# Kernel tuning notes

Hardware: AMD Instinct MI355X
Metric: run time of the kernel (lower is better)

The kernel has to match this reference:

```python
import jax, jax.numpy as jnp
import numpy as np

B, N, D, H = 16, 256, 1024, 8
DK = D // H
WAVE_LEN = 1000.0


def box_relational_embedding(boxes):
    # boxes: (B, N, 4) as (x_min, y_min, x_max, y_max)
    x_min, y_min, x_max, y_max = jnp.split(boxes, 4, axis=-1)  # each (B, N, 1)
    cx = (x_min + x_max) * 0.5
    cy = (y_min + y_max) * 0.5
    w = (x_max - x_min) + 1.0
    h = (y_max - y_min) + 1.0
    # pairwise deltas (B, N, N); row i = query box, col j = key box
    delta_x = jnp.log(jnp.clip(jnp.abs((cx - jnp.swapaxes(cx, -2, -1)) / w), 1e-3, None))
    delta_y = jnp.log(jnp.clip(jnp.abs((cy - jnp.swapaxes(cy, -2, -1)) / h), 1e-3, None))
    delta_w = jnp.log(w / jnp.swapaxes(w, -2, -1))
    delta_h = jnp.log(h / jnp.swapaxes(h, -2, -1))
    pos = jnp.stack([delta_x, delta_y, delta_w, delta_h], axis=-1)  # (B, N, N, 4)
    # sinusoidal expansion: dim_g = 64 -> 8 frequencies per delta
    feat_range = jnp.arange(8, dtype=pos.dtype) / 8.0
    dim_mat = 1.0 / (WAVE_LEN ** feat_range)  # (8,)
    mul = (100.0 * pos)[..., None] * dim_mat  # (B, N, N, 4, 8)
    mul = mul.reshape(pos.shape[:3] + (32,))
    return jnp.concatenate([jnp.sin(mul), jnp.cos(mul)], axis=-1)  # (B, N, N, 64)


def setup_inputs() -> dict:
    key = jax.random.key(0)
    ks = jax.random.split(key, 12)
    x = jax.random.normal(ks[0], (B, N, D), dtype=jnp.float32)
    # valid boxes: x_max > x_min, y_max > y_min
    xy = jax.random.uniform(ks[1], (B, N, 2), dtype=jnp.float32) * 100.0
    wh = jax.random.uniform(ks[2], (B, N, 2), dtype=jnp.float32) * 50.0 + 1.0
    boxes = jnp.concatenate([xy, xy + wh], axis=-1)
    s = 1.0 / np.sqrt(D)
    Wq = jax.random.normal(ks[3], (D, D), dtype=jnp.float32) * s
    Wk = jax.random.normal(ks[4], (D, D), dtype=jnp.float32) * s
    Wv = jax.random.normal(ks[5], (D, D), dtype=jnp.float32) * s
    Wo = jax.random.normal(ks[6], (D, D), dtype=jnp.float32) * s
    bq = jnp.zeros((D,), jnp.float32)
    bk = jnp.zeros((D,), jnp.float32)
    bv = jnp.zeros((D,), jnp.float32)
    bo = jnp.zeros((D,), jnp.float32)
    Wg = jax.random.normal(ks[7], (H, 64), dtype=jnp.float32) * (1.0 / 8.0)  # 8 per-head (64->1) linears
    bg = jnp.zeros((H,), jnp.float32)
    return {"x": x, "boxes": boxes, "Wq": Wq, "bq": bq, "Wk": Wk, "bk": bk,
            "Wv": Wv, "bv": bv, "Wo": Wo, "bo": bo, "Wg": Wg, "bg": bg}


def reference(x, boxes, Wq, bq, Wk, bk, Wv, bv, Wo, bo, Wg, bg):
    emb = box_relational_embedding(boxes)  # (B, N, N, 64)
    # per-head geometric weights, ReLU'd: (B, H, N, N)
    geo = jax.nn.relu(jnp.einsum('bnmg,hg->bhnm', emb, Wg) + bg[None, :, None, None])
    q = (x @ Wq + bq).reshape(B, N, H, DK).transpose(0, 2, 1, 3)  # (B, H, N, DK)
    k = (x @ Wk + bk).reshape(B, N, H, DK).transpose(0, 2, 1, 3)
    v = (x @ Wv + bv).reshape(B, N, H, DK).transpose(0, 2, 1, 3)
    scores = jnp.einsum('bhnd,bhmd->bhnm', q, k) / np.sqrt(DK)
    w_mn = jax.nn.softmax(jnp.log(jnp.clip(geo, 1e-6, None)) + scores, axis=-1)
    out = jnp.einsum('bhnm,bhmd->bhnd', w_mn, v)  # (B, H, N, DK)
    out = out.transpose(0, 2, 1, 3).reshape(B, N, D)
    return out @ Wo + bo
```

## Files before the change

kernel.cpp:

```cpp
#include <hip/hip_runtime.h>

#define Bb 16
#define Nn 256
#define Dd 1024
#define Hh 8
#define DKk 128

typedef unsigned short u16;
typedef __attribute__((ext_vector_type(8))) short bfrag;
typedef __attribute__((ext_vector_type(4))) float f4;

#define MFMA16(a, b, c) __builtin_amdgcn_mfma_f32_16x16x32_bf16((a), (b), (c), 0, 0, 0)

__device__ __forceinline__ u16 f2b(float f) {
  unsigned int u = __builtin_bit_cast(unsigned int, f);
  u += 0x7fffu + ((u >> 16) & 1u);
  return (u16)(u >> 16);
}

typedef __attribute__((address_space(1))) void GV;
typedef __attribute__((address_space(3))) void LV;
__device__ __forceinline__ void gload16(const void* g, void* l) {
  __builtin_amdgcn_global_load_lds((GV*)g, (LV*)l, 16, 0, 0);
}

__global__ __launch_bounds__(256) void cast_x_kernel(const float* __restrict__ x,
                                                     u16* __restrict__ xb) {
  const int i = blockIdx.x * 256 + threadIdx.x;
  const float4 v = ((const float4*)x)[i];
  union { u16 u[4]; unsigned long long ll; } p;
  p.u[0] = f2b(v.x); p.u[1] = f2b(v.y); p.u[2] = f2b(v.z); p.u[3] = f2b(v.w);
  ((unsigned long long*)xb)[i] = p.ll;
}

__global__ __launch_bounds__(256) void transpose_w_kernel(
    const float* __restrict__ Wq, const float* __restrict__ Wk,
    const float* __restrict__ Wv, const float* __restrict__ Wo,
    u16* __restrict__ wqkvt, u16* __restrict__ wot) {
  __shared__ float t[32][33];
  const int bid = blockIdx.x;
  const int which = bid >> 10;
  const int tr = (bid >> 5) & 31;
  const int tc = bid & 31;
  const float* W = which == 0 ? Wq : which == 1 ? Wk : which == 2 ? Wv : Wo;
  u16* dst = (which == 3) ? wot : (wqkvt + (long long)which * 1024 * 1024);
  const int tx = threadIdx.x & 31, ty = threadIdx.x >> 5;
#pragma unroll
  for (int rr = 0; rr < 4; rr++)
    t[ty + rr * 8][tx] = W[(tr * 32 + ty + rr * 8) * 1024 + tc * 32 + tx];
  __syncthreads();
#pragma unroll
  for (int rr = 0; rr < 4; rr++)
    dst[(tc * 32 + ty + rr * 8) * 1024 + tr * 32 + tx] = f2b(t[tx][ty + rr * 8]);
}

__global__ __launch_bounds__(256) void transpose_v_kernel(const u16* __restrict__ v,
                                                          u16* __restrict__ vT) {
  __shared__ u16 t[32][33];
  const int bid = blockIdx.x;
  const int bh = bid >> 5;
  const int kt = (bid >> 2) & 7;
  const int ct = bid & 3;
  const u16* src = v + (long long)bh * Nn * DKk;
  u16* dst = vT + (long long)bh * DKk * Nn;
  const int tx = threadIdx.x & 31, ty = threadIdx.x >> 5;
#pragma unroll
  for (int rr = 0; rr < 4; rr++)
    t[ty + rr * 8][tx] = src[(kt * 32 + ty + rr * 8) * DKk + ct * 32 + tx];
  __syncthreads();
#pragma unroll
  for (int rr = 0; rr < 4; rr++)
    dst[(ct * 32 + ty + rr * 8) * Nn + kt * 32 + tx] = t[tx][ty + rr * 8];
}

__global__ __launch_bounds__(256) void geo_kernel(const float* __restrict__ boxes,
                                                  const float* __restrict__ Wg,
                                                  const float* __restrict__ bg,
                                                  float* __restrict__ logg) {
  __shared__ float wg_s[512];
  __shared__ float bg_s[8];
  const int tid = threadIdx.x;
  wg_s[tid] = Wg[tid];
  wg_s[tid + 256] = Wg[tid + 256];
  if (tid < 8) bg_s[tid] = bg[tid];
  __syncthreads();
  const int bid = blockIdx.x;
  const int b = bid >> 8, i = bid & 255;
  const int j = tid;
  const float4 bi4 = ((const float4*)boxes)[b * 256 + i];
  const float4 bj4 = ((const float4*)boxes)[b * 256 + j];
  const float cxi = (bi4.x + bi4.z) * 0.5f, cyi = (bi4.y + bi4.w) * 0.5f;
  const float wi = bi4.z - bi4.x + 1.f, hi = bi4.w - bi4.y + 1.f;
  const float cxj = (bj4.x + bj4.z) * 0.5f, cyj = (bj4.y + bj4.w) * 0.5f;
  const float wj = bj4.z - bj4.x + 1.f, hj = bj4.w - bj4.y + 1.f;
  float pos[4];
  pos[0] = __logf(fmaxf(fabsf((cxi - cxj) / wi), 1e-3f));
  pos[1] = __logf(fmaxf(fabsf((cyi - cyj) / hi), 1e-3f));
  pos[2] = __logf(wi / wj);
  pos[3] = __logf(hi / hj);
  const float dimm[8] = {1.0f, 0.42169650342f, 0.177827941f, 0.0749894209f,
                         0.0316227766f, 0.01333521432f, 0.00562341325f, 0.00237137371f};
  float sv[32], cv[32];
#pragma unroll
  for (int d = 0; d < 4; d++)
#pragma unroll
    for (int f = 0; f < 8; f++) {
      const float ang = 100.f * pos[d] * dimm[f];
      __sincosf(ang, &sv[d * 8 + f], &cv[d * 8 + f]);
    }
  const long long base = ((long long)(b * 8) * 256 + i) * 256 + j;
#pragma unroll
  for (int h = 0; h < 8; h++) {
    float a = bg_s[h];
#pragma unroll
    for (int t = 0; t < 32; t++)
      a = fmaf(sv[t], wg_s[h * 64 + t], fmaf(cv[t], wg_s[h * 64 + 32 + t], a));
    logg[base + (long long)h * 65536] = __logf(fmaxf(a, 1e-6f));
  }
}

template <int MODE>
__global__ __launch_bounds__(256) void gemm128(
    const u16* __restrict__ A, const u16* __restrict__ Bt,
    const float* __restrict__ b0, const float* __restrict__ b1,
    const float* __restrict__ b2, u16* __restrict__ oq, u16* __restrict__ ok,
    u16* __restrict__ ov, float* __restrict__ co, int M, int Np, int K) {
  __shared__ u16 As[128 * 32];
  __shared__ u16 Bs[128 * 32];
  const int tilesN = Np >> 7;
  const int bm = blockIdx.x / tilesN, bn = blockIdx.x - bm * tilesN;
  const int m0 = bm << 7, n0 = bn << 7;
  const int tid = threadIdx.x, lane = tid & 63, w = tid >> 6;
  const int wr = w >> 1, wc = w & 1;
  const int fr = lane & 15, fq = lane >> 4;

  f4 acc[4][4];
#pragma unroll
  for (int i = 0; i < 4; i++)
#pragma unroll
    for (int j = 0; j < 4; j++) acc[i][j] = (f4){0.f, 0.f, 0.f, 0.f};

  const int srow = (w << 5) + (lane >> 2);
  const int skel = (lane & 3) << 3;
  const u16* Ag0 = A + (long long)(m0 + srow) * K + skel;
  const u16* Ag1 = Ag0 + 16 * K;
  const u16* Bg0 = Bt + (long long)(n0 + srow) * K + skel;
  const u16* Bg1 = Bg0 + 16 * K;
  u16* Al0 = As + (w << 5) * 32;
  u16* Al1 = Al0 + 16 * 32;
  u16* Bl0 = Bs + (w << 5) * 32;
  u16* Bl1 = Bl0 + 16 * 32;

  for (int k0 = 0; k0 < K; k0 += 32) {
    __syncthreads();
    gload16(Ag0 + k0, Al0);
    gload16(Ag1 + k0, Al1);
    gload16(Bg0 + k0, Bl0);
    gload16(Bg1 + k0, Bl1);
    __syncthreads();
    bfrag av[4], bv[4];
#pragma unroll
    for (int i = 0; i < 4; i++)
      av[i] = *(const bfrag*)(As + ((wr << 6) + (i << 4) + fr) * 32 + (fq << 3));
#pragma unroll
    for (int j = 0; j < 4; j++)
      bv[j] = *(const bfrag*)(Bs + ((wc << 6) + (j << 4) + fr) * 32 + (fq << 3));
#pragma unroll
    for (int i = 0; i < 4; i++)
#pragma unroll
      for (int j = 0; j < 4; j++) acc[i][j] = MFMA16(av[i], bv[j], acc[i][j]);
  }

  if constexpr (MODE == 0) {
#pragma unroll
    for (int j = 0; j < 4; j++) {
      const int n = n0 + (wc << 6) + (j << 4) + fr;
      const int which = n >> 10;
      const int hh = (n >> 7) & 7;
      const int dk = n & 127;
      const float bia = (which == 0 ? b0 : which == 1 ? b1 : b2)[n & 1023];
      u16* dst = (which == 0 ? oq : which == 1 ? ok : ov);
      const float scl = (which == 0) ? 0.08838834764831845f : 1.0f;
#pragma unroll
      for (int i = 0; i < 4; i++)
#pragma unroll
        for (int r = 0; r < 4; r++) {
          const int m = m0 + (wr << 6) + (i << 4) + (fq << 2) + r;
          const int bidx = m >> 8, itok = m & 255;
          dst[((long long)(bidx * 8 + hh) * 256 + itok) * 128 + dk] =
              f2b((acc[i][j][r] + bia) * scl);
        }
    }
  } else {
#pragma unroll
    for (int i = 0; i < 4; i++)
#pragma unroll
      for (int j = 0; j < 4; j++) {
        const int n = n0 + (wc << 6) + (j << 4) + fr;
        const float bia = b0[n];
#pragma unroll
        for (int r = 0; r < 4; r++) {
          const int m = m0 + (wr << 6) + (i << 4) + (fq << 2) + r;
          co[(long long)m * Np + n] = acc[i][j][r] + bia;
        }
      }
  }
}

__global__ __launch_bounds__(256) void attn_kernel(
    const u16* __restrict__ q, const u16* __restrict__ k,
    const u16* __restrict__ vT, const float* __restrict__ logg,
    u16* __restrict__ aout) {
  __shared__ u16 plds[4][16][272];
  const int bid = blockIdx.x;
  const int qt = bid & 3;
  const int bh = bid >> 2;
  const int tid = threadIdx.x, lane = tid & 63, w = tid >> 6;
  const int fr = lane & 15, fq = lane >> 4;
  const int i0 = qt * 64 + w * 16;
  const u16* qp = q + (long long)bh * Nn * DKk;
  const u16* kp = k + (long long)bh * Nn * DKk;
  const u16* vp = vT + (long long)bh * DKk * Nn;
  const float* gg = logg + (long long)bh * Nn * Nn;

  bfrag qf[4];
#pragma unroll
  for (int ks = 0; ks < 4; ks++)
    qf[ks] = *(const bfrag*)(qp + (i0 + fr) * DKk + ks * 32 + fq * 8);

  f4 s[16];
#pragma unroll
  for (int j = 0; j < 16; j++) s[j] = (f4){0.f, 0.f, 0.f, 0.f};
#pragma unroll
  for (int j = 0; j < 16; j++)
#pragma unroll
    for (int ks = 0; ks < 4; ks++) {
      bfrag kf = *(const bfrag*)(kp + (j * 16 + fr) * DKk + ks * 32 + fq * 8);
      s[j] = MFMA16(qf[ks], kf, s[j]);
    }

#pragma unroll
  for (int j = 0; j < 16; j++)
#pragma unroll
    for (int r = 0; r < 4; r++)
      s[j][r] += gg[(i0 + fq * 4 + r) * Nn + j * 16 + fr];

  float sm[4];
#pragma unroll
  for (int r = 0; r < 4; r++) {
    float m = s[0][r];
#pragma unroll
    for (int j = 1; j < 16; j++) m = fmaxf(m, s[j][r]);
    m = fmaxf(m, __shfl_xor(m, 1));
    m = fmaxf(m, __shfl_xor(m, 2));
    m = fmaxf(m, __shfl_xor(m, 4));
    m = fmaxf(m, __shfl_xor(m, 8));
    float t = 0.f;
#pragma unroll
    for (int j = 0; j < 16; j++) {
      const float p = __expf(s[j][r] - m);
      s[j][r] = p;
      t += p;
    }
    t += __shfl_xor(t, 1);
    t += __shfl_xor(t, 2);
    t += __shfl_xor(t, 4);
    t += __shfl_xor(t, 8);
    sm[r] = t;
  }

#pragma unroll
  for (int j = 0; j < 16; j++)
#pragma unroll
    for (int r = 0; r < 4; r++)
      plds[w][fq * 4 + r][j * 16 + fr] = f2b(s[j][r]);
  __syncthreads();

  f4 o[8];
#pragma unroll
  for (int d = 0; d < 8; d++) o[d] = (f4){0.f, 0.f, 0.f, 0.f};
#pragma unroll
  for (int jt = 0; jt < 8; jt++) {
    bfrag pf = *(const bfrag*)(&plds[w][fr][jt * 32 + fq * 8]);
#pragma unroll
    for (int d = 0; d < 8; d++) {
      bfrag vf = *(const bfrag*)(vp + (d * 16 + fr) * Nn + jt * 32 + fq * 8);
      o[d] = MFMA16(pf, vf, o[d]);
    }
  }

  const int b = bh >> 3, h = bh & 7;
  float inv[4];
#pragma unroll
  for (int r = 0; r < 4; r++) inv[r] = 1.0f / sm[r];
#pragma unroll
  for (int d = 0; d < 8; d++)
#pragma unroll
    for (int r = 0; r < 4; r++) {
      const int row = i0 + fq * 4 + r;
      const int dk = d * 16 + fr;
      aout[((long long)(b * 256 + row)) * 1024 + h * 128 + dk] =
          f2b(o[d][r] * inv[r]);
    }
}

extern "C" void kernel_launch(void* const* d_in, const int* in_sizes, int n_in,
                              void* d_out, int out_size, void* d_ws, size_t ws_size,
                              hipStream_t stream) {
  (void)in_sizes; (void)n_in; (void)out_size; (void)ws_size;
  const float* x = (const float*)d_in[0];
  const float* boxes = (const float*)d_in[1];
  const float* Wq = (const float*)d_in[2];
  const float* bq = (const float*)d_in[3];
  const float* Wk = (const float*)d_in[4];
  const float* bk = (const float*)d_in[5];
  const float* Wv = (const float*)d_in[6];
  const float* bv = (const float*)d_in[7];
  const float* Wo = (const float*)d_in[8];
  const float* bo = (const float*)d_in[9];
  const float* Wg = (const float*)d_in[10];
  const float* bg = (const float*)d_in[11];
  float* out = (float*)d_out;

  char* ws = (char*)d_ws;
  u16* xb    = (u16*)(ws);
  u16* wqkvt = (u16*)(ws + (8ll << 20));
  u16* wot   = (u16*)(ws + (14ll << 20));
  u16* qb    = (u16*)(ws + (16ll << 20));
  u16* kb    = (u16*)(ws + (24ll << 20));
  u16* vb    = (u16*)(ws + (32ll << 20));
  u16* vtb   = (u16*)(ws + (40ll << 20));
  float* logg = (float*)(ws + (48ll << 20));
  u16* aout  = (u16*)(ws + (80ll << 20));

  cast_x_kernel<<<4096, 256, 0, stream>>>(x, xb);
  transpose_w_kernel<<<4096, 256, 0, stream>>>(Wq, Wk, Wv, Wo, wqkvt, wot);
  geo_kernel<<<4096, 256, 0, stream>>>(boxes, Wg, bg, logg);
  gemm128<0><<<32 * 24, 256, 0, stream>>>(xb, wqkvt, bq, bk, bv, qb, kb, vb,
                                          nullptr, 4096, 3072, 1024);
  transpose_v_kernel<<<4096, 256, 0, stream>>>(vb, vtb);
  attn_kernel<<<512, 256, 0, stream>>>(qb, kb, vtb, logg, aout);
  gemm128<1><<<32 * 8, 256, 0, stream>>>(aout, wot, bo, nullptr, nullptr, nullptr,
                                         nullptr, nullptr, out, 4096, 1024, 1024);
}
```

Before: 251.5 us.

## Store geometric log-bias in fp16 and split attention keys across wave pairs

Measured after the change: 233.9 us. 7.0% less time.

```diff
diff --git a/kernel.cpp b/kernel.cpp
--- a/kernel.cpp
+++ b/kernel.cpp
@@ -1,4 +1,5 @@
 #include <hip/hip_runtime.h>
+#include <hip/hip_fp16.h>
 
 #define Bb 16
 #define Nn 256
@@ -76,7 +77,7 @@
 __global__ __launch_bounds__(256) void geo_kernel(const float* __restrict__ boxes,
                                                   const float* __restrict__ Wg,
                                                   const float* __restrict__ bg,
-                                                  float* __restrict__ logg) {
+                                                  __half* __restrict__ logg) {
   __shared__ float wg_s[512];
   __shared__ float bg_s[8];
   const int tid = threadIdx.x;
@@ -115,7 +116,7 @@
 #pragma unroll
     for (int t = 0; t < 32; t++)
       a = fmaf(sv[t], wg_s[h * 64 + t], fmaf(cv[t], wg_s[h * 64 + 32 + t], a));
-    logg[base + (long long)h * 65536] = __logf(fmaxf(a, 1e-6f));
+    logg[base + (long long)h * 65536] = __float2half(__logf(fmaxf(a, 1e-6f)));
   }
 }
 
@@ -207,57 +208,74 @@
   }
 }
 
-__global__ __launch_bounds__(256) void attn_kernel(
+__global__ __launch_bounds__(256, 4) void attn_kernel(
     const u16* __restrict__ q, const u16* __restrict__ k,
-    const u16* __restrict__ vT, const float* __restrict__ logg,
+    const u16* __restrict__ vT, const __half* __restrict__ logg,
     u16* __restrict__ aout) {
-  __shared__ u16 plds[4][16][272];
+  __shared__ __align__(16) char smem[16384 + 17408 + 256];
+  __half* ggs = (__half*)smem;
+  u16* plds = (u16*)(smem + 16384);
+  float* mbuf = (float*)(smem + 16384);
+  float* mlb = (float*)(smem + 16384 + 17408);
+
   const int bid = blockIdx.x;
-  const int qt = bid & 3;
-  const int bh = bid >> 2;
+  const int qt = bid & 7;
+  const int bh = bid >> 3;
   const int tid = threadIdx.x, lane = tid & 63, w = tid >> 6;
+  const int rg = w >> 1, kh = w & 1;
   const int fr = lane & 15, fq = lane >> 4;
-  const int i0 = qt * 64 + w * 16;
+  const int i0 = qt * 32 + rg * 16;
+
   const u16* qp = q + (long long)bh * Nn * DKk;
-  const u16* kp = k + (long long)bh * Nn * DKk;
+  const u16* kp = k + (long long)bh * Nn * DKk + kh * 128 * DKk;
   const u16* vp = vT + (long long)bh * DKk * Nn;
-  const float* gg = logg + (long long)bh * Nn * Nn;
+  const __half* gp = logg + (long long)bh * Nn * Nn;
+
+  __half* ggw = ggs + w * (16 * 128);
+  {
+    const int r4 = lane >> 4, c8 = lane & 15;
+#pragma unroll
+    for (int t = 0; t < 4; t++)
+      gload16(gp + (i0 + t * 4 + r4) * Nn + kh * 128 + c8 * 8, ggw + t * 512);
+  }
 
   bfrag qf[4];
 #pragma unroll
   for (int ks = 0; ks < 4; ks++)
     qf[ks] = *(const bfrag*)(qp + (i0 + fr) * DKk + ks * 32 + fq * 8);
 
-  f4 s[16];
-#pragma unroll
-  for (int j = 0; j < 16; j++) s[j] = (f4){0.f, 0.f, 0.f, 0.f};
-#pragma unroll
-  for (int j = 0; j < 16; j++)
+  f4 s[8];
+#pragma unroll
+  for (int j = 0; j < 8; j++) s[j] = (f4){0.f, 0.f, 0.f, 0.f};
+#pragma unroll
+  for (int j = 0; j < 8; j++)
 #pragma unroll
     for (int ks = 0; ks < 4; ks++) {
       bfrag kf = *(const bfrag*)(kp + (j * 16 + fr) * DKk + ks * 32 + fq * 8);
       s[j] = MFMA16(qf[ks], kf, s[j]);
     }
 
-#pragma unroll
-  for (int j = 0; j < 16; j++)
+  asm volatile("s_waitcnt vmcnt(0)" ::: "memory");
+
+#pragma unroll
+  for (int j = 0; j < 8; j++)
 #pragma unroll
     for (int r = 0; r < 4; r++)
-      s[j][r] += gg[(i0 + fq * 4 + r) * Nn + j * 16 + fr];
-
-  float sm[4];
+      s[j][r] += __half2float(ggw[(fq * 4 + r) * 128 + j * 16 + fr]);
+
+  float mr[4], lr[4];
 #pragma unroll
   for (int r = 0; r < 4; r++) {
     float m = s[0][r];
 #pragma unroll
-    for (int j = 1; j < 16; j++) m = fmaxf(m, s[j][r]);
+    for (int j = 1; j < 8; j++) m = fmaxf(m, s[j][r]);
     m = fmaxf(m, __shfl_xor(m, 1));
     m = fmaxf(m, __shfl_xor(m, 2));
     m = fmaxf(m, __shfl_xor(m, 4));
     m = fmaxf(m, __shfl_xor(m, 8));
     float t = 0.f;
 #pragma unroll
-    for (int j = 0; j < 16; j++) {
+    for (int j = 0; j < 8; j++) {
       const float p = __expf(s[j][r] - m);
       s[j][r] = p;
       t += p;
@@ -266,42 +284,72 @@
     t += __shfl_xor(t, 2);
     t += __shfl_xor(t, 4);
     t += __shfl_xor(t, 8);
-    sm[r] = t;
-  }
-
-#pragma unroll
-  for (int j = 0; j < 16; j++)
+    mr[r] = m;
+    lr[r] = t;
+  }
+
+  u16* pw = plds + w * (16 * 136);
+#pragma unroll
+  for (int j = 0; j < 8; j++)
 #pragma unroll
     for (int r = 0; r < 4; r++)
-      plds[w][fq * 4 + r][j * 16 + fr] = f2b(s[j][r]);
+      pw[(fq * 4 + r) * 136 + j * 16 + fr] = f2b(s[j][r]);
   __syncthreads();
 
   f4 o[8];
 #pragma unroll
   for (int d = 0; d < 8; d++) o[d] = (f4){0.f, 0.f, 0.f, 0.f};
 #pragma unroll
-  for (int jt = 0; jt < 8; jt++) {
-    bfrag pf = *(const bfrag*)(&plds[w][fr][jt * 32 + fq * 8]);
+  for (int jt = 0; jt < 4; jt++) {
+    bfrag pf = *(const bfrag*)(pw + fr * 136 + jt * 32 + fq * 8);
 #pragma unroll
     for (int d = 0; d < 8; d++) {
-      bfrag vf = *(const bfrag*)(vp + (d * 16 + fr) * Nn + jt * 32 + fq * 8);
+      bfrag vf = *(const bfrag*)(vp + (d * 16 + fr) * Nn + kh * 128 + jt * 32 + fq * 8);
       o[d] = MFMA16(pf, vf, o[d]);
     }
   }
-
-  const int b = bh >> 3, h = bh & 7;
-  float inv[4];
-#pragma unroll
-  for (int r = 0; r < 4; r++) inv[r] = 1.0f / sm[r];
-#pragma unroll
-  for (int d = 0; d < 8; d++)
+  __syncthreads();
+
+  if (kh) {
+    float* ob = mbuf + rg * (16 * 132);
+#pragma unroll
+    for (int d = 0; d < 8; d++)
+#pragma unroll
+      for (int r = 0; r < 4; r++)
+        ob[(fq * 4 + r) * 132 + d * 16 + fr] = o[d][r];
+    if (fr == 0)
+#pragma unroll
+      for (int r = 0; r < 4; r++) {
+        mlb[rg * 32 + (fq * 4 + r) * 2] = mr[r];
+        mlb[rg * 32 + (fq * 4 + r) * 2 + 1] = lr[r];
+      }
+  }
+  __syncthreads();
+
+  if (!kh) {
+    const int b = bh >> 3, h = bh & 7;
+    float a0[4], a1[4], invl[4];
 #pragma unroll
     for (int r = 0; r < 4; r++) {
-      const int row = i0 + fq * 4 + r;
-      const int dk = d * 16 + fr;
-      aout[((long long)(b * 256 + row)) * 1024 + h * 128 + dk] =
-          f2b(o[d][r] * inv[r]);
-    }
+      const float m1 = mlb[rg * 32 + (fq * 4 + r) * 2];
+      const float l1 = mlb[rg * 32 + (fq * 4 + r) * 2 + 1];
+      const float m = fmaxf(mr[r], m1);
+      a0[r] = __expf(mr[r] - m);
+      a1[r] = __expf(m1 - m);
+      invl[r] = 1.0f / (lr[r] * a0[r] + l1 * a1[r]);
+    }
+    const float* ob = mbuf + rg * (16 * 132);
+#pragma unroll
+    for (int d = 0; d < 8; d++)
+#pragma unroll
+      for (int r = 0; r < 4; r++) {
+        const float o1 = ob[(fq * 4 + r) * 132 + d * 16 + fr];
+        const float val = (o[d][r] * a0[r] + o1 * a1[r]) * invl[r];
+        const int row = i0 + fq * 4 + r;
+        const int dk = d * 16 + fr;
+        aout[((long long)(b * 256 + row)) * 1024 + h * 128 + dk] = f2b(val);
+      }
+  }
 }
 
 extern "C" void kernel_launch(void* const* d_in, const int* in_sizes, int n_in,
@@ -330,8 +378,8 @@
   u16* kb    = (u16*)(ws + (24ll << 20));
   u16* vb    = (u16*)(ws + (32ll << 20));
   u16* vtb   = (u16*)(ws + (40ll << 20));
-  float* logg = (float*)(ws + (48ll << 20));
-  u16* aout  = (u16*)(ws + (80ll << 20));
+  __half* logg = (__half*)(ws + (48ll << 20));
+  u16* aout  = (u16*)(ws + (64ll << 20));
 
   cast_x_kernel<<<4096, 256, 0, stream>>>(x, xb);
   transpose_w_kernel<<<4096, 256, 0, stream>>>(Wq, Wk, Wv, Wo, wqkvt, wot);
@@ -339,7 +387,7 @@
   gemm128<0><<<32 * 24, 256, 0, stream>>>(xb, wqkvt, bq, bk, bv, qb, kb, vb,
                                           nullptr, 4096, 3072, 1024);
   transpose_v_kernel<<<4096, 256, 0, stream>>>(vb, vtb);
-  attn_kernel<<<512, 256, 0, stream>>>(qb, kb, vtb, logg, aout);
+  attn_kernel<<<1024, 256, 0, stream>>>(qb, kb, vtb, logg, aout);
   gemm128<1><<<32 * 8, 256, 0, stream>>>(aout, wot, bo, nullptr, nullptr, nullptr,
                                          nullptr, nullptr, out, 4096, 1024, 1024);
 }
```
